# Kernel tuning notes

Measured on AMD Instinct MI355X. Metric: run time of the kernel, lower is better.

The kernel has to match this reference:

```python
import jax, jax.numpy as jnp
import numpy as np

B, S = 16, 1024
D_MODEL, N_MEL = 256, 80
IN_DIM = D_MODEL * (((N_MEL - 1) // 2 - 1) // 2)  # 4864
G, V, CV_DIM = 2, 320, 256


def setup_inputs() -> dict:
    key = jax.random.key(0)
    k1, k2, k3 = jax.random.split(key, 3)
    hidden_states = jax.random.normal(k1, (B, S, IN_DIM), dtype=jnp.float32)
    W = jax.random.normal(k2, (IN_DIM, G * V), dtype=jnp.float32) / np.sqrt(IN_DIM)
    b = jnp.zeros((G * V,), dtype=jnp.float32)
    codevectors = jax.random.normal(k3, (1, G * V, CV_DIM // G), dtype=jnp.float32)
    return {"hidden_states": hidden_states, "W": W, "b": b,
            "codevectors": codevectors, "num_groups": G}


def reference(hidden_states, W, b, codevectors, num_groups):
    bsz, seq, _ = hidden_states.shape
    logits = hidden_states @ W + b                      # (B, S, G*V)
    gv = logits.shape[-1]
    nvars = gv // num_groups
    flat = logits.reshape(bsz * seq, num_groups, nvars)  # (BS, G, V)
    idx = jnp.argmax(flat, axis=-1)                      # (BS, G) int
    # one-hot codevector probs (eval / hard argmax branch)
    probs = jax.nn.one_hot(idx, nvars, dtype=logits.dtype)  # (BS, G, V)
    marginal = probs.mean(axis=0)                        # (G, V)
    perplexity = jnp.exp(-jnp.sum(marginal * jnp.log(marginal + 1e-7), axis=-1)).sum()
    # weighted sum over codebook == gather of selected codevector per group
    cv = codevectors.reshape(num_groups, nvars, -1)      # (G, V, Dg)
    gathered = cv[jnp.arange(num_groups)[None, :], idx]  # (BS, G, Dg)
    out = gathered.reshape(bsz, seq, -1)                 # (B, S, codevector_dim)
    return (out, perplexity)
```

## Files before the change

kernel.cpp:

```cpp
#include <hip/hip_runtime.h>
#include <stdint.h>

#define M_TOT 16384
#define K_TOT 4864
#define N_TOT 640
#define GRP   2
#define NV    320
#define CVD   128

#define BM 128
#define BN 320
#define BK 32
#define KITERS (K_TOT / BK)

#define MARGIN 2.0e-3f

typedef __attribute__((ext_vector_type(8))) short short8;
typedef __attribute__((ext_vector_type(4))) float f32x4;

#define WS_FLAGCNT  0
#define WS_COUNTS   256
#define WS_FLAGLIST 4096
#define WS_PACKED   (4096 + 262144)
#define WS_WT       (1u << 20)

__device__ __forceinline__ unsigned int mono_u32(float f) {
    unsigned int b = __float_as_uint(f);
    return b ^ ((unsigned int)((int)b >> 31) | 0x80000000u);
}
__device__ __forceinline__ unsigned short f2bf(float x) {
    unsigned int u = __float_as_uint(x);
    return (unsigned short)((u + 0x7fffu + ((u >> 16) & 1u)) >> 16);
}
__device__ __forceinline__ float bf2f(unsigned short h) {
    return __uint_as_float(((unsigned int)h) << 16);
}
__device__ __forceinline__ void gld16(const void* g, void* l) {
    __builtin_amdgcn_global_load_lds(
        (const __attribute__((address_space(1))) unsigned int*)g,
        (__attribute__((address_space(3))) unsigned int*)l, 16, 0, 0);
}

__global__ __launch_bounds__(256)
void convert_wt(const float* __restrict__ W, unsigned short* __restrict__ wt)
{
    __shared__ float sW[64][68];
    const int k0 = blockIdx.x * 64;
    const int n0 = blockIdx.y * 64;
    const int tid = threadIdx.x;
    for (int l = tid; l < 64 * 16; l += 256) {
        int kr = l >> 4, nc = (l & 15) * 4;
        float4 v = *(const float4*)(W + (size_t)(k0 + kr) * N_TOT + n0 + nc);
        sW[kr][nc] = v.x; sW[kr][nc + 1] = v.y; sW[kr][nc + 2] = v.z; sW[kr][nc + 3] = v.w;
    }
    __syncthreads();
    unsigned short* whi = wt;
    unsigned short* wlo = wt + (size_t)N_TOT * K_TOT;
    for (int l = tid; l < 64 * 8; l += 256) {
        int nr = l >> 3, ko = (l & 7) * 8;
        union { short8 v; unsigned short u[8]; } hu, lu;
#pragma unroll
        for (int j = 0; j < 8; ++j) {
            float x = sW[ko + j][nr];
            unsigned short hb = f2bf(x);
            hu.u[j] = hb;
            lu.u[j] = f2bf(x - bf2f(hb));
        }
        size_t off = (size_t)(n0 + nr) * K_TOT + k0 + ko;
        *(short8*)(whi + off) = hu.v;
        *(short8*)(wlo + off) = lu.v;
    }
}

__device__ __forceinline__ void stage_b(const unsigned short* __restrict__ wt,
                                        short* sBbuf, int bx, int kk, int tid)
{
#pragma unroll
    for (int r = 0; r < 5; ++r) {
        int c = r * 512 + tid;
        int half = (c >= 1280) ? 1 : 0;
        int cc = c - half * 1280;
        int row = cc >> 2, oct = cc & 3;
        const unsigned short* gp = wt + (size_t)half * N_TOT * K_TOT
            + (size_t)(bx * NV + row) * K_TOT + kk + ((oct ^ (row & 3)) << 3);
        gld16(gp, sBbuf + (size_t)c * 8);
    }
}

__global__ __launch_bounds__(512, 2)
void gemm_mfma(const float* __restrict__ A, const unsigned short* __restrict__ wt,
               const float* __restrict__ bias,
               unsigned long long* __restrict__ packed,
               unsigned int* __restrict__ flagcnt, unsigned int* __restrict__ flaglist)
{
    __shared__ short sA[2][2][BM][BK];
    __shared__ short sB[2][2][BN][BK];
    __shared__ uint4 sRed[BM][4];

    const int tid  = threadIdx.x;
    const int L    = tid & 63;
    const int w    = tid >> 6;
    const int quad = L >> 4;
    const int lrow = L & 15;
    const int wrow = w >> 2;
    const int wcol = w & 3;
    const int bx   = blockIdx.x;
    const int m0   = blockIdx.y * BM;
    const int octr = quad ^ (L & 3);

    const int arow = tid >> 2;
    const int aoct = tid & 3;
    const float* Ap = A + (size_t)(m0 + arow) * K_TOT + aoct * 8;
    const int aswz = ((aoct ^ (arow & 3)) << 3);

    f32x4 acc[4][5];
#pragma unroll
    for (int i = 0; i < 4; ++i)
#pragma unroll
        for (int j = 0; j < 5; ++j) acc[i][j] = (f32x4){0.f, 0.f, 0.f, 0.f};

    {
        stage_b(wt, &sB[0][0][0][0], bx, 0, tid);
        float4 a0 = *(const float4*)(Ap);
        float4 a1 = *(const float4*)(Ap + 4);
        union { short8 v; unsigned short u[8]; } hu, lu;
        float xs[8] = {a0.x, a0.y, a0.z, a0.w, a1.x, a1.y, a1.z, a1.w};
#pragma unroll
        for (int j = 0; j < 8; ++j) {
            unsigned short hb = f2bf(xs[j]);
            hu.u[j] = hb; lu.u[j] = f2bf(xs[j] - bf2f(hb));
        }
        *(short8*)&sA[0][0][arow][aswz] = hu.v;
        *(short8*)&sA[0][1][arow][aswz] = lu.v;
    }
    __syncthreads();

    int k0 = 0;
    for (int it = 0; it < KITERS; ++it) {
        const int buf = it & 1;
        const int kn  = k0 + BK;
        float4 a0, a1;
        const bool more = (it + 1 < KITERS);
        if (more) {
            stage_b(wt, &sB[buf ^ 1][0][0][0], bx, kn, tid);
            a0 = *(const float4*)(Ap + kn);
            a1 = *(const float4*)(Ap + kn + 4);
        }
        short8 ah[4], al[4];
#pragma unroll
        for (int fi = 0; fi < 4; ++fi) {
            int mloc = wrow * 64 + fi * 16 + lrow;
            ah[fi] = *(const short8*)&sA[buf][0][mloc][octr * 8];
            al[fi] = *(const short8*)&sA[buf][1][mloc][octr * 8];
        }
#pragma unroll
        for (int fj = 0; fj < 5; ++fj) {
            int nloc = wcol * 80 + fj * 16 + lrow;
            short8 bh = *(const short8*)&sB[buf][0][nloc][octr * 8];
            short8 bl = *(const short8*)&sB[buf][1][nloc][octr * 8];
#pragma unroll
            for (int fi = 0; fi < 4; ++fi) {
                acc[fi][fj] = __builtin_amdgcn_mfma_f32_16x16x32_bf16(ah[fi], bh, acc[fi][fj], 0, 0, 0);
                acc[fi][fj] = __builtin_amdgcn_mfma_f32_16x16x32_bf16(ah[fi], bl, acc[fi][fj], 0, 0, 0);
                acc[fi][fj] = __builtin_amdgcn_mfma_f32_16x16x32_bf16(al[fi], bh, acc[fi][fj], 0, 0, 0);
            }
        }
        if (more) {
            union { short8 v; unsigned short u[8]; } hu, lu;
            float xs[8] = {a0.x, a0.y, a0.z, a0.w, a1.x, a1.y, a1.z, a1.w};
#pragma unroll
            for (int j = 0; j < 8; ++j) {
                unsigned short hb = f2bf(xs[j]);
                hu.u[j] = hb; lu.u[j] = f2bf(xs[j] - bf2f(hb));
            }
            *(short8*)&sA[buf ^ 1][0][arow][aswz] = hu.v;
            *(short8*)&sA[buf ^ 1][1][arow][aswz] = lu.v;
        }
        __syncthreads();
        k0 = kn;
    }

    float bs[5];
#pragma unroll
    for (int fj = 0; fj < 5; ++fj)
        bs[fj] = bias[bx * NV + wcol * 80 + fj * 16 + lrow];

#pragma unroll
    for (int fi = 0; fi < 4; ++fi) {
#pragma unroll
        for (int r = 0; r < 4; ++r) {
            unsigned long long pv = 0; float v1 = 0.f, v2 = -3.4e38f;
#pragma unroll
            for (int fj = 0; fj < 5; ++fj) {
                float v = acc[fi][fj][r] + bs[fj];
                int cig = wcol * 80 + fj * 16 + lrow;
                unsigned long long p = ((unsigned long long)mono_u32(v) << 32)
                                     | (unsigned int)(NV - 1 - cig);
                if (fj == 0) { pv = p; v1 = v; }
                else if (p > pv) { v2 = v1; v1 = v; pv = p; }
                else { v2 = fmaxf(v2, v); }
            }
#pragma unroll
            for (int msk = 1; msk < 16; msk <<= 1) {
                unsigned long long opv = __shfl_xor(pv, msk);
                float ov1 = __shfl_xor(v1, msk);
                float ov2 = __shfl_xor(v2, msk);
                if (opv > pv) { v2 = fmaxf(v1, ov2); v1 = ov1; pv = opv; }
                else          { v2 = fmaxf(v2, ov1); }
            }
            if (lrow == 0) {
                int row_blk = wrow * 64 + fi * 16 + quad * 4 + r;
                uint4 e;
                e.x = (unsigned int)(pv & 0xFFFFFFFFull);
                e.y = (unsigned int)(pv >> 32);
                e.z = __float_as_uint(v2);
                e.w = __float_as_uint(v1);
                sRed[row_blk][wcol] = e;
            }
        }
    }
    __syncthreads();

    if (tid < BM) {
        unsigned long long pv = 0; float v1 = -3.4e38f, v2 = -3.4e38f;
#pragma unroll
        for (int wc = 0; wc < 4; ++wc) {
            uint4 e = sRed[tid][wc];
            unsigned long long opv = ((unsigned long long)e.y << 32) | e.x;
            float ov1 = __uint_as_float(e.w), ov2 = __uint_as_float(e.z);
            if (opv > pv) { v2 = fmaxf(v1, ov2); v1 = ov1; pv = opv; }
            else          { v2 = fmaxf(v2, ov1); }
        }
        packed[(size_t)(m0 + tid) * GRP + bx] = pv;
        if (v1 - v2 <= MARGIN) {
            unsigned int slot = atomicAdd(flagcnt, 1u);
            flaglist[slot] = ((unsigned int)(m0 + tid) << 1) | (unsigned int)bx;
        }
    }
}

__global__ __launch_bounds__(320)
void recheck(const float* __restrict__ A, const float* __restrict__ W,
             const float* __restrict__ bias,
             const unsigned int* __restrict__ flagcnt,
             const unsigned int* __restrict__ flaglist,
             unsigned long long* __restrict__ packed)
{
    __shared__ float  sAr[K_TOT];
    __shared__ float4 sPart[320];
    __shared__ float  sVals[NV];
    const int tid = threadIdx.x;
    const unsigned int cnt = *flagcnt;
    const int kseg = tid / 80, c4 = tid % 80;
    for (unsigned int i = blockIdx.x; i < cnt; i += gridDim.x) {
        unsigned int item = flaglist[i];
        int row = (int)(item >> 1), g = (int)(item & 1);
        __syncthreads();
        for (int l = tid; l < K_TOT / 4; l += 320)
            *(float4*)&sAr[l * 4] = *(const float4*)(A + (size_t)row * K_TOT + l * 4);
        __syncthreads();
        float4 acc = {0.f, 0.f, 0.f, 0.f};
        const float* wp = W + (size_t)(kseg * 1216) * N_TOT + g * NV + c4 * 4;
        const float* ap = sAr + kseg * 1216;
        for (int k = 0; k < 1216; ++k) {
            float a = ap[k];
            float4 wv = *(const float4*)(wp + (size_t)k * N_TOT);
            acc.x = fmaf(a, wv.x, acc.x);
            acc.y = fmaf(a, wv.y, acc.y);
            acc.z = fmaf(a, wv.z, acc.z);
            acc.w = fmaf(a, wv.w, acc.w);
        }
        sPart[tid] = acc;
        __syncthreads();
        if (tid < 80) {
            float4 s = {0.f, 0.f, 0.f, 0.f};
#pragma unroll
            for (int ks = 0; ks < 4; ++ks) {
                float4 p = sPart[ks * 80 + tid];
                s.x += p.x; s.y += p.y; s.z += p.z; s.w += p.w;
            }
            float4 bb = *(const float4*)(bias + g * NV + tid * 4);
            sVals[tid * 4 + 0] = s.x + bb.x;
            sVals[tid * 4 + 1] = s.y + bb.y;
            sVals[tid * 4 + 2] = s.z + bb.z;
            sVals[tid * 4 + 3] = s.w + bb.w;
        }
        __syncthreads();
        if (tid == 0) {
            float best = sVals[0]; int bi = 0;
            for (int c = 1; c < NV; ++c)
                if (sVals[c] > best) { best = sVals[c]; bi = c; }
            packed[(size_t)row * GRP + g] =
                ((unsigned long long)mono_u32(best) << 32) | (unsigned int)(NV - 1 - bi);
        }
    }
}

__global__ __launch_bounds__(256)
void gather_hist(const unsigned long long* __restrict__ packed,
                 const float* __restrict__ cv,
                 float* __restrict__ out, int* __restrict__ counts)
{
    const int m = blockIdx.x;
    const int t = threadIdx.x;
    const int g = t >> 7;
    const unsigned long long p = packed[(size_t)m * GRP + g];
    const int idx = (NV - 1) - (int)(p & 0xFFFFFFFFull);
    const int c = t & 127;
    out[(size_t)m * (GRP * CVD) + t] = cv[((size_t)g * NV + idx) * CVD + c];
    if (c == 0) atomicAdd(&counts[g * NV + idx], 1);
}

__global__ void perplexity_k(const int* __restrict__ counts, float* __restrict__ outp)
{
    __shared__ float sred[GRP * NV];
    const int t = threadIdx.x;
    const float marg = (float)counts[t] * (1.0f / (float)M_TOT);
    sred[t] = marg * logf(marg + 1e-7f);
    __syncthreads();
    if (t < GRP) {
        float s = 0.f;
        for (int i = 0; i < NV; ++i) s += sred[t * NV + i];
        sred[t] = expf(-s);
    }
    __syncthreads();
    if (t == 0) outp[0] = sred[0] + sred[1];
}

extern "C" void kernel_launch(void* const* d_in, const int* in_sizes, int n_in,
                              void* d_out, int out_size, void* d_ws, size_t ws_size,
                              hipStream_t stream)
{
    const float* A    = (const float*)d_in[0];
    const float* Wm   = (const float*)d_in[1];
    const float* bias = (const float*)d_in[2];
    const float* cv   = (const float*)d_in[3];

    float* out = (float*)d_out;
    float* ppl = out + (size_t)M_TOT * (GRP * CVD);

    char* ws = (char*)d_ws;
    unsigned int*       flagcnt  = (unsigned int*)(ws + WS_FLAGCNT);
    int*                counts   = (int*)(ws + WS_COUNTS);
    unsigned int*       flaglist = (unsigned int*)(ws + WS_FLAGLIST);
    unsigned long long* packed   = (unsigned long long*)(ws + WS_PACKED);
    unsigned short*     wt       = (unsigned short*)(ws + WS_WT);

    hipMemsetAsync(d_ws, 0, 4096, stream);
    convert_wt<<<dim3(76, 10), 256, 0, stream>>>(Wm, wt);
    gemm_mfma<<<dim3(2, 128), 512, 0, stream>>>(A, wt, bias, packed, flagcnt, flaglist);
    recheck<<<256, 320, 0, stream>>>(A, Wm, bias, flagcnt, flaglist, packed);
    gather_hist<<<M_TOT, 256, 0, stream>>>(packed, cv, out, counts);
    perplexity_k<<<1, GRP * NV, 0, stream>>>(counts, ppl);
}
```

Measured before the change: 808.2 us.

## Interleave hi/lo bf16 LDS layout, batch recheck rows, tighten margin, grid-stride gather

Stores the hi and lo bf16 halves of A and B tiles in one 64-short row, using an 8-way XOR swizzle, so LDS reads and global-to-LDS loads use a wider conflict-free pattern. The recheck kernel now handles four flagged rows per block, sharing each W load across them, and splits the flag lists per group. The near-tie margin is reduced so fewer rows are rechecked in fp32. The gather kernel becomes grid-stride over 4096 blocks. The smaller margin risks missing true argmax ties that the split-bf16 error could flip, and the shared memory in recheck grows by four times.

Measured after the change: 881.1 us. +9.0%, slower.

```diff
diff --git a/kernel.cpp b/kernel.cpp
--- a/kernel.cpp
+++ b/kernel.cpp
@@ -13,7 +13,7 @@
 #define BK 32
 #define KITERS (K_TOT / BK)
 
-#define MARGIN 2.0e-3f
+#define MARGIN 5.0e-4f
 
 typedef __attribute__((ext_vector_type(8))) short short8;
 typedef __attribute__((ext_vector_type(4))) float f32x4;
@@ -21,6 +21,7 @@
 #define WS_FLAGCNT  0
 #define WS_COUNTS   256
 #define WS_FLAGLIST 4096
+#define FLAGCAP     32768
 #define WS_PACKED   (4096 + 262144)
 #define WS_WT       (1u << 20)
 
@@ -78,11 +79,11 @@
 #pragma unroll
     for (int r = 0; r < 5; ++r) {
         int c = r * 512 + tid;
-        int half = (c >= 1280) ? 1 : 0;
-        int cc = c - half * 1280;
-        int row = cc >> 2, oct = cc & 3;
+        int row = c >> 3, slot = c & 7;
+        int sv = slot ^ (row & 7);
+        int half = sv >> 2, oct = sv & 3;
         const unsigned short* gp = wt + (size_t)half * N_TOT * K_TOT
-            + (size_t)(bx * NV + row) * K_TOT + kk + ((oct ^ (row & 3)) << 3);
+            + (size_t)(bx * NV + row) * K_TOT + kk + (oct << 3);
         gld16(gp, sBbuf + (size_t)c * 8);
     }
 }
@@ -93,8 +94,8 @@
                unsigned long long* __restrict__ packed,
                unsigned int* __restrict__ flagcnt, unsigned int* __restrict__ flaglist)
 {
-    __shared__ short sA[2][2][BM][BK];
-    __shared__ short sB[2][2][BN][BK];
+    __shared__ short sA[2][BM][64];
+    __shared__ short sB[2][BN][64];
     __shared__ uint4 sRed[BM][4];
 
     const int tid  = threadIdx.x;
@@ -106,12 +107,15 @@
     const int wcol = w & 3;
     const int bx   = blockIdx.x;
     const int m0   = blockIdx.y * BM;
-    const int octr = quad ^ (L & 3);
+
+    const int sh = (quad ^ (lrow & 7)) << 3;
+    const int sl = ((4 | quad) ^ (lrow & 7)) << 3;
 
     const int arow = tid >> 2;
     const int aoct = tid & 3;
     const float* Ap = A + (size_t)(m0 + arow) * K_TOT + aoct * 8;
-    const int aswz = ((aoct ^ (arow & 3)) << 3);
+    const int sHa = (aoct ^ (arow & 7)) << 3;
+    const int sLa = ((4 | aoct) ^ (arow & 7)) << 3;
 
     f32x4 acc[4][5];
 #pragma unroll
@@ -120,9 +124,9 @@
         for (int j = 0; j < 5; ++j) acc[i][j] = (f32x4){0.f, 0.f, 0.f, 0.f};
 
     {
-        stage_b(wt, &sB[0][0][0][0], bx, 0, tid);
         float4 a0 = *(const float4*)(Ap);
         float4 a1 = *(const float4*)(Ap + 4);
+        stage_b(wt, &sB[0][0][0], bx, 0, tid);
         union { short8 v; unsigned short u[8]; } hu, lu;
         float xs[8] = {a0.x, a0.y, a0.z, a0.w, a1.x, a1.y, a1.z, a1.w};
 #pragma unroll
@@ -130,8 +134,8 @@
             unsigned short hb = f2bf(xs[j]);
             hu.u[j] = hb; lu.u[j] = f2bf(xs[j] - bf2f(hb));
         }
-        *(short8*)&sA[0][0][arow][aswz] = hu.v;
-        *(short8*)&sA[0][1][arow][aswz] = lu.v;
+        *(short8*)&sA[0][arow][sHa] = hu.v;
+        *(short8*)&sA[0][arow][sLa] = lu.v;
     }
     __syncthreads();
 
@@ -142,22 +146,22 @@
         float4 a0, a1;
         const bool more = (it + 1 < KITERS);
         if (more) {
-            stage_b(wt, &sB[buf ^ 1][0][0][0], bx, kn, tid);
             a0 = *(const float4*)(Ap + kn);
             a1 = *(const float4*)(Ap + kn + 4);
+            stage_b(wt, &sB[buf ^ 1][0][0], bx, kn, tid);
         }
         short8 ah[4], al[4];
 #pragma unroll
         for (int fi = 0; fi < 4; ++fi) {
             int mloc = wrow * 64 + fi * 16 + lrow;
-            ah[fi] = *(const short8*)&sA[buf][0][mloc][octr * 8];
-            al[fi] = *(const short8*)&sA[buf][1][mloc][octr * 8];
+            ah[fi] = *(const short8*)&sA[buf][mloc][sh];
+            al[fi] = *(const short8*)&sA[buf][mloc][sl];
         }
 #pragma unroll
         for (int fj = 0; fj < 5; ++fj) {
             int nloc = wcol * 80 + fj * 16 + lrow;
-            short8 bh = *(const short8*)&sB[buf][0][nloc][octr * 8];
-            short8 bl = *(const short8*)&sB[buf][1][nloc][octr * 8];
+            short8 bh = *(const short8*)&sB[buf][nloc][sh];
+            short8 bl = *(const short8*)&sB[buf][nloc][sl];
 #pragma unroll
             for (int fi = 0; fi < 4; ++fi) {
                 acc[fi][fj] = __builtin_amdgcn_mfma_f32_16x16x32_bf16(ah[fi], bh, acc[fi][fj], 0, 0, 0);
@@ -173,8 +177,8 @@
                 unsigned short hb = f2bf(xs[j]);
                 hu.u[j] = hb; lu.u[j] = f2bf(xs[j] - bf2f(hb));
             }
-            *(short8*)&sA[buf ^ 1][0][arow][aswz] = hu.v;
-            *(short8*)&sA[buf ^ 1][1][arow][aswz] = lu.v;
+            *(short8*)&sA[buf ^ 1][arow][sHa] = hu.v;
+            *(short8*)&sA[buf ^ 1][arow][sLa] = lu.v;
         }
         __syncthreads();
         k0 = kn;
@@ -233,12 +237,13 @@
         }
         packed[(size_t)(m0 + tid) * GRP + bx] = pv;
         if (v1 - v2 <= MARGIN) {
-            unsigned int slot = atomicAdd(flagcnt, 1u);
-            flaglist[slot] = ((unsigned int)(m0 + tid) << 1) | (unsigned int)bx;
-        }
-    }
-}
-
+            unsigned int slot = atomicAdd(&flagcnt[bx], 1u);
+            flaglist[bx * FLAGCAP + slot] = (unsigned int)(m0 + tid);
+        }
+    }
+}
+
+#define RCH_IPB 4
 __global__ __launch_bounds__(320)
 void recheck(const float* __restrict__ A, const float* __restrict__ W,
              const float* __restrict__ bias,
@@ -246,51 +251,76 @@
              const unsigned int* __restrict__ flaglist,
              unsigned long long* __restrict__ packed)
 {
-    __shared__ float  sAr[K_TOT];
-    __shared__ float4 sPart[320];
-    __shared__ float  sVals[NV];
+    __shared__ float  sAr[RCH_IPB][K_TOT];
+    __shared__ float4 sPart[RCH_IPB][320];
+    __shared__ float  sVals[RCH_IPB][NV];
+    __shared__ int    sRow[RCH_IPB];
     const int tid = threadIdx.x;
-    const unsigned int cnt = *flagcnt;
+    const int g   = blockIdx.x & 1;
+    const unsigned int cnt = flagcnt[g];
+    const unsigned int* list = flaglist + g * FLAGCAP;
     const int kseg = tid / 80, c4 = tid % 80;
-    for (unsigned int i = blockIdx.x; i < cnt; i += gridDim.x) {
-        unsigned int item = flaglist[i];
-        int row = (int)(item >> 1), g = (int)(item & 1);
-        __syncthreads();
-        for (int l = tid; l < K_TOT / 4; l += 320)
-            *(float4*)&sAr[l * 4] = *(const float4*)(A + (size_t)row * K_TOT + l * 4);
-        __syncthreads();
-        float4 acc = {0.f, 0.f, 0.f, 0.f};
+    for (unsigned int base = (unsigned int)(blockIdx.x >> 1) * RCH_IPB; base < cnt;
+         base += (unsigned int)(gridDim.x >> 1) * RCH_IPB) {
+        const unsigned int nit = (cnt - base < (unsigned int)RCH_IPB)
+                               ? (cnt - base) : (unsigned int)RCH_IPB;
+        __syncthreads();
+        if (tid < RCH_IPB) {
+            unsigned int src = base + (unsigned int)tid;
+            if (src >= cnt) src = base;
+            sRow[tid] = (int)list[src];
+        }
+        __syncthreads();
+        for (int l = tid; l < RCH_IPB * (K_TOT / 4); l += 320) {
+            int j = l / (K_TOT / 4), off = l - j * (K_TOT / 4);
+            *(float4*)&sAr[j][off * 4] =
+                *(const float4*)(A + (size_t)sRow[j] * K_TOT + off * 4);
+        }
+        __syncthreads();
+        float4 ac0 = {0.f,0.f,0.f,0.f}, ac1 = {0.f,0.f,0.f,0.f};
+        float4 ac2 = {0.f,0.f,0.f,0.f}, ac3 = {0.f,0.f,0.f,0.f};
         const float* wp = W + (size_t)(kseg * 1216) * N_TOT + g * NV + c4 * 4;
-        const float* ap = sAr + kseg * 1216;
+        const float* a0p = &sAr[0][kseg * 1216];
+        const float* a1p = &sAr[1][kseg * 1216];
+        const float* a2p = &sAr[2][kseg * 1216];
+        const float* a3p = &sAr[3][kseg * 1216];
         for (int k = 0; k < 1216; ++k) {
-            float a = ap[k];
             float4 wv = *(const float4*)(wp + (size_t)k * N_TOT);
-            acc.x = fmaf(a, wv.x, acc.x);
-            acc.y = fmaf(a, wv.y, acc.y);
-            acc.z = fmaf(a, wv.z, acc.z);
-            acc.w = fmaf(a, wv.w, acc.w);
-        }
-        sPart[tid] = acc;
+            float av0 = a0p[k], av1 = a1p[k], av2 = a2p[k], av3 = a3p[k];
+            ac0.x = fmaf(av0, wv.x, ac0.x); ac0.y = fmaf(av0, wv.y, ac0.y);
+            ac0.z = fmaf(av0, wv.z, ac0.z); ac0.w = fmaf(av0, wv.w, ac0.w);
+            ac1.x = fmaf(av1, wv.x, ac1.x); ac1.y = fmaf(av1, wv.y, ac1.y);
+            ac1.z = fmaf(av1, wv.z, ac1.z); ac1.w = fmaf(av1, wv.w, ac1.w);
+            ac2.x = fmaf(av2, wv.x, ac2.x); ac2.y = fmaf(av2, wv.y, ac2.y);
+            ac2.z = fmaf(av2, wv.z, ac2.z); ac2.w = fmaf(av2, wv.w, ac2.w);
+            ac3.x = fmaf(av3, wv.x, ac3.x); ac3.y = fmaf(av3, wv.y, ac3.y);
+            ac3.z = fmaf(av3, wv.z, ac3.z); ac3.w = fmaf(av3, wv.w, ac3.w);
+        }
+        sPart[0][tid] = ac0; sPart[1][tid] = ac1;
+        sPart[2][tid] = ac2; sPart[3][tid] = ac3;
         __syncthreads();
         if (tid < 80) {
-            float4 s = {0.f, 0.f, 0.f, 0.f};
-#pragma unroll
-            for (int ks = 0; ks < 4; ++ks) {
-                float4 p = sPart[ks * 80 + tid];
-                s.x += p.x; s.y += p.y; s.z += p.z; s.w += p.w;
-            }
-            float4 bb = *(const float4*)(bias + g * NV + tid * 4);
-            sVals[tid * 4 + 0] = s.x + bb.x;
-            sVals[tid * 4 + 1] = s.y + bb.y;
-            sVals[tid * 4 + 2] = s.z + bb.z;
-            sVals[tid * 4 + 3] = s.w + bb.w;
-        }
-        __syncthreads();
-        if (tid == 0) {
-            float best = sVals[0]; int bi = 0;
+#pragma unroll
+            for (int j = 0; j < RCH_IPB; ++j) {
+                float4 s = {0.f, 0.f, 0.f, 0.f};
+#pragma unroll
+                for (int ks = 0; ks < 4; ++ks) {
+                    float4 p = sPart[j][ks * 80 + tid];
+                    s.x += p.x; s.y += p.y; s.z += p.z; s.w += p.w;
+                }
+                float4 bb = *(const float4*)(bias + g * NV + tid * 4);
+                sVals[j][tid * 4 + 0] = s.x + bb.x;
+                sVals[j][tid * 4 + 1] = s.y + bb.y;
+                sVals[j][tid * 4 + 2] = s.z + bb.z;
+                sVals[j][tid * 4 + 3] = s.w + bb.w;
+            }
+        }
+        __syncthreads();
+        if (tid < (int)nit) {
+            float best = sVals[tid][0]; int bi = 0;
             for (int c = 1; c < NV; ++c)
-                if (sVals[c] > best) { best = sVals[c]; bi = c; }
-            packed[(size_t)row * GRP + g] =
+                if (sVals[tid][c] > best) { best = sVals[tid][c]; bi = c; }
+            packed[(size_t)sRow[tid] * GRP + g] =
                 ((unsigned long long)mono_u32(best) << 32) | (unsigned int)(NV - 1 - bi);
         }
     }
@@ -301,14 +331,15 @@
                  const float* __restrict__ cv,
                  float* __restrict__ out, int* __restrict__ counts)
 {
-    const int m = blockIdx.x;
     const int t = threadIdx.x;
     const int g = t >> 7;
-    const unsigned long long p = packed[(size_t)m * GRP + g];
-    const int idx = (NV - 1) - (int)(p & 0xFFFFFFFFull);
     const int c = t & 127;
-    out[(size_t)m * (GRP * CVD) + t] = cv[((size_t)g * NV + idx) * CVD + c];
-    if (c == 0) atomicAdd(&counts[g * NV + idx], 1);
+    for (int m = blockIdx.x; m < M_TOT; m += gridDim.x) {
+        const unsigned long long p = packed[(size_t)m * GRP + g];
+        const int idx = (NV - 1) - (int)(p & 0xFFFFFFFFull);
+        out[(size_t)m * (GRP * CVD) + t] = cv[((size_t)g * NV + idx) * CVD + c];
+        if (c == 0) atomicAdd(&counts[g * NV + idx], 1);
+    }
 }
 
 __global__ void perplexity_k(const int* __restrict__ counts, float* __restrict__ outp)
@@ -350,6 +381,6 @@
     convert_wt<<<dim3(76, 10), 256, 0, stream>>>(Wm, wt);
     gemm_mfma<<<dim3(2, 128), 512, 0, stream>>>(A, wt, bias, packed, flagcnt, flaglist);
     recheck<<<256, 320, 0, stream>>>(A, Wm, bias, flagcnt, flaglist, packed);
-    gather_hist<<<M_TOT, 256, 0, stream>>>(packed, cv, out, counts);
+    gather_hist<<<4096, 256, 0, stream>>>(packed, cv, out, counts);
     perplexity_k<<<1, GRP * NV, 0, stream>>>(counts, ppl);
 }
```
